# Performance work log

Measured on AMD Instinct MI355X. Metric: run time of the kernel, lower is better.

The kernel has to match this reference:

```python
import jax, jax.numpy as jnp
import numpy as np

DIM = 768
N_HEADS = 12
HEAD_DIM = DIM // N_HEADS
BATCH = 2
SEQ = 4096


def setup_inputs() -> dict:
    key = jax.random.key(0)
    ks = jax.random.split(key, 9)
    s = 1.0 / np.sqrt(DIM)
    return {
        "x": jax.random.normal(ks[0], (BATCH, SEQ, DIM), dtype=jnp.float32),
        "Wq": jax.random.normal(ks[1], (DIM, DIM), dtype=jnp.float32) * s,
        "bq": jax.random.normal(ks[2], (DIM,), dtype=jnp.float32) * s,
        "Wk": jax.random.normal(ks[3], (DIM, DIM), dtype=jnp.float32) * s,
        "bk": jax.random.normal(ks[4], (DIM,), dtype=jnp.float32) * s,
        "Wv": jax.random.normal(ks[5], (DIM, DIM), dtype=jnp.float32) * s,
        "bv": jax.random.normal(ks[6], (DIM,), dtype=jnp.float32) * s,
        "Wo": jax.random.normal(ks[7], (DIM, DIM), dtype=jnp.float32) * s,
        "bo": jax.random.normal(ks[8], (DIM,), dtype=jnp.float32) * s,
    }


def reference(x, Wq, bq, Wk, bk, Wv, bv, Wo, bo):
    B, S, D = x.shape
    scale = 1.0 / np.sqrt(HEAD_DIM).astype(np.float32)
    # projections: [B,S,D] -> [B,H,S,Hd]
    def split_heads(t):
        return t.reshape(B, S, N_HEADS, HEAD_DIM).transpose(0, 2, 1, 3)
    q = split_heads(x @ Wq + bq)
    k = split_heads(x @ Wk + bk)
    v = split_heads(x @ Wv + bv)
    # full score matrix [B,H,S,S] as in the original (memory-bound)
    scores = jnp.einsum("bhqd,bhkd->bhqk", q, k) * scale
    attn = jax.nn.softmax(scores, axis=-1)
    out = jnp.einsum("bhqk,bhkd->bhqd", attn, v)
    out = out.transpose(0, 2, 1, 3).reshape(B, S, D)
    return out @ Wo + bo
```

## Files before the change

### kernel.cpp

```cpp
#include <hip/hip_runtime.h>
#include <hip/hip_bf16.h>
#include <math.h>

#define D_MODEL 768
#define NH 12
#define HD 64
#define BATCH 2
#define SEQ 4096
#define NROWS (BATCH * SEQ)

#define QSCALE 0.18033688011112042f

typedef __attribute__((ext_vector_type(8))) short short8;
typedef __attribute__((ext_vector_type(4))) short short4v;
typedef __attribute__((ext_vector_type(4))) float f32x4;
typedef __attribute__((ext_vector_type(16))) float f32x16;

__device__ inline unsigned short f2bf(float f) {
    __hip_bfloat16 h = __float2bfloat16(f);
    return *reinterpret_cast<unsigned short*>(&h);
}

__device__ __forceinline__ void async_ld16(const unsigned short* g, unsigned short* l) {
    __builtin_amdgcn_global_load_lds(
        (const __attribute__((address_space(1))) void*)g,
        (__attribute__((address_space(3))) void*)l, 16, 0, 0);
}

__global__ __launch_bounds__(256) void convert_x_k(
    const float* __restrict__ x, unsigned short* __restrict__ xb)
{
    size_t i = ((size_t)blockIdx.x * 256 + threadIdx.x) * 8;
    float4 a = *(const float4*)(x + i);
    float4 b = *(const float4*)(x + i + 4);
    short8 o;
    o[0] = (short)f2bf(a.x); o[1] = (short)f2bf(a.y);
    o[2] = (short)f2bf(a.z); o[3] = (short)f2bf(a.w);
    o[4] = (short)f2bf(b.x); o[5] = (short)f2bf(b.y);
    o[6] = (short)f2bf(b.z); o[7] = (short)f2bf(b.w);
    *(short8*)(xb + i) = o;
}

__global__ __launch_bounds__(256) void convert_wt_k(
    const float* __restrict__ Wq, const float* __restrict__ Wk,
    const float* __restrict__ Wv, const float* __restrict__ Wo,
    unsigned short* __restrict__ wt)
{
    const float* W = (blockIdx.z == 0) ? Wq : (blockIdx.z == 1) ? Wk
                   : (blockIdx.z == 2) ? Wv : Wo;
    unsigned short* dst = wt + (size_t)blockIdx.z * D_MODEL * D_MODEL;
    __shared__ float tile[64][65];
    const int k0 = blockIdx.x * 64, n0 = blockIdx.y * 64;
    const int t = threadIdx.x;
    const int r = t >> 2, seg = t & 3;
    const float* src = W + (size_t)(k0 + r) * D_MODEL + n0 + seg * 16;
    #pragma unroll
    for (int i = 0; i < 4; ++i) {
        float4 v = *(const float4*)(src + i * 4);
        tile[r][seg * 16 + i * 4 + 0] = v.x;
        tile[r][seg * 16 + i * 4 + 1] = v.y;
        tile[r][seg * 16 + i * 4 + 2] = v.z;
        tile[r][seg * 16 + i * 4 + 3] = v.w;
    }
    __syncthreads();
    unsigned short* d = dst + (size_t)(n0 + r) * D_MODEL + k0 + seg * 16;
    short8 o0, o1;
    #pragma unroll
    for (int j = 0; j < 8; ++j) o0[j] = (short)f2bf(tile[seg * 16 + j][r]);
    #pragma unroll
    for (int j = 0; j < 8; ++j) o1[j] = (short)f2bf(tile[seg * 16 + 8 + j][r]);
    *(short8*)(d) = o0;
    *(short8*)(d + 8) = o1;
}

__global__ __launch_bounds__(256) void qkv_mfma_k(
    const unsigned short* __restrict__ xb,
    const unsigned short* __restrict__ wt,
    const float* __restrict__ bq, const float* __restrict__ bk,
    const float* __restrict__ bv,
    unsigned short* __restrict__ qb,
    unsigned short* __restrict__ kb,
    unsigned short* __restrict__ vtb)
{
    __shared__ unsigned short As[128][64];
    __shared__ unsigned short Bs[64][64];
    const int z = blockIdx.z;
    const unsigned short* Wt = wt + (size_t)z * D_MODEL * D_MODEL;
    const float* bias = (z == 0) ? bq : (z == 1) ? bk : bv;
    const int t = threadIdx.x;
    const int w = t >> 6, lane = t & 63, quad = lane >> 4, col = lane & 15;
    const int r0 = blockIdx.x * 128;
    const int c0 = blockIdx.y * 64;

    f32x4 acc[2][4] = {};

    for (int kk = 0; kk < D_MODEL; kk += 64) {
        __syncthreads();
        #pragma unroll
        for (int j = 0; j < 4; ++j) {
            int c = (w * 4 + j) * 64 + lane;
            async_ld16(xb + (size_t)(r0 + (c >> 3)) * D_MODEL + kk + (c & 7) * 8,
                       &As[0][0] + (size_t)c * 8);
        }
        #pragma unroll
        for (int j = 0; j < 2; ++j) {
            int c = (w * 2 + j) * 64 + lane;
            async_ld16(Wt + (size_t)(c0 + (c >> 3)) * D_MODEL + kk + (c & 7) * 8,
                       &Bs[0][0] + (size_t)c * 8);
        }
        __syncthreads();
        #pragma unroll
        for (int ks = 0; ks < 2; ++ks) {
            short8 af[2], bf[4];
            af[0] = *(const short8*)&As[w * 32 + col][ks * 32 + quad * 8];
            af[1] = *(const short8*)&As[w * 32 + 16 + col][ks * 32 + quad * 8];
            #pragma unroll
            for (int nt = 0; nt < 4; ++nt)
                bf[nt] = *(const short8*)&Bs[nt * 16 + col][ks * 32 + quad * 8];
            #pragma unroll
            for (int mt = 0; mt < 2; ++mt)
                #pragma unroll
                for (int nt = 0; nt < 4; ++nt)
                    acc[mt][nt] = __builtin_amdgcn_mfma_f32_16x16x32_bf16(
                        af[mt], bf[nt], acc[mt][nt], 0, 0, 0);
        }
    }

    const int h = blockIdx.y;
    #pragma unroll
    for (int nt = 0; nt < 4; ++nt) {
        const float bv_ = bias[c0 + nt * 16 + col];
        const int hd = nt * 16 + col;
        #pragma unroll
        for (int mt = 0; mt < 2; ++mt) {
            #pragma unroll
            for (int reg = 0; reg < 4; ++reg) {
                int r = r0 + w * 32 + mt * 16 + quad * 4 + reg;
                int b = r >> 12, s = r & (SEQ - 1);
                float val = acc[mt][nt][reg] + bv_;
                size_t bh = (size_t)(b * NH + h);
                if (z == 0)
                    qb[(bh * SEQ + s) * HD + hd] = f2bf(val * QSCALE);
                else if (z == 1)
                    kb[(bh * SEQ + s) * HD + hd] = f2bf(val);
                else
                    vtb[(bh * HD + hd) * SEQ + s] = f2bf(val);
            }
        }
    }
}

__global__ __launch_bounds__(256) void out_mfma_k(
    const unsigned short* __restrict__ ab,
    const unsigned short* __restrict__ wot,
    const float* __restrict__ bo,
    float* __restrict__ out)
{
    __shared__ unsigned short As[128][64];
    __shared__ unsigned short Bs[64][64];
    const int t = threadIdx.x;
    const int w = t >> 6, lane = t & 63, quad = lane >> 4, col = lane & 15;
    const int r0 = blockIdx.x * 128;
    const int c0 = blockIdx.y * 64;

    f32x4 acc[2][4] = {};

    for (int kk = 0; kk < D_MODEL; kk += 64) {
        __syncthreads();
        #pragma unroll
        for (int j = 0; j < 4; ++j) {
            int c = (w * 4 + j) * 64 + lane;
            async_ld16(ab + (size_t)(r0 + (c >> 3)) * D_MODEL + kk + (c & 7) * 8,
                       &As[0][0] + (size_t)c * 8);
        }
        #pragma unroll
        for (int j = 0; j < 2; ++j) {
            int c = (w * 2 + j) * 64 + lane;
            async_ld16(wot + (size_t)(c0 + (c >> 3)) * D_MODEL + kk + (c & 7) * 8,
                       &Bs[0][0] + (size_t)c * 8);
        }
        __syncthreads();
        #pragma unroll
        for (int ks = 0; ks < 2; ++ks) {
            short8 af[2], bf[4];
            af[0] = *(const short8*)&As[w * 32 + col][ks * 32 + quad * 8];
            af[1] = *(const short8*)&As[w * 32 + 16 + col][ks * 32 + quad * 8];
            #pragma unroll
            for (int nt = 0; nt < 4; ++nt)
                bf[nt] = *(const short8*)&Bs[nt * 16 + col][ks * 32 + quad * 8];
            #pragma unroll
            for (int mt = 0; mt < 2; ++mt)
                #pragma unroll
                for (int nt = 0; nt < 4; ++nt)
                    acc[mt][nt] = __builtin_amdgcn_mfma_f32_16x16x32_bf16(
                        af[mt], bf[nt], acc[mt][nt], 0, 0, 0);
        }
    }

    #pragma unroll
    for (int nt = 0; nt < 4; ++nt) {
        const float bv_ = bo[c0 + nt * 16 + col];
        #pragma unroll
        for (int mt = 0; mt < 2; ++mt) {
            #pragma unroll
            for (int reg = 0; reg < 4; ++reg) {
                int r = r0 + w * 32 + mt * 16 + quad * 4 + reg;
                out[(size_t)r * D_MODEL + c0 + nt * 16 + col] = acc[mt][nt][reg] + bv_;
            }
        }
    }
}

__global__ __launch_bounds__(256) void flash_mfma_k(
    const unsigned short* __restrict__ qb,
    const unsigned short* __restrict__ kb,
    const unsigned short* __restrict__ vtb,
    unsigned short* __restrict__ ab)
{
    __shared__ unsigned short Ks[64][66];
    __shared__ unsigned short Vts[64][66];
    __shared__ unsigned short Ps[4][32][66];

    const int t = threadIdx.x;
    const int w = t >> 6, lane = t & 63;
    const int l31 = lane & 31, hi = lane >> 5;
    const int q0 = blockIdx.x * 128;
    const int h = blockIdx.y, b = blockIdx.z;
    const size_t bh = (size_t)b * NH + h;
    const unsigned short* qg = qb + bh * SEQ * HD;
    const unsigned short* kg = kb + bh * SEQ * HD;
    const unsigned short* vg = vtb + bh * HD * SEQ;

    short8 qf[4];
    {
        const unsigned short* src = qg + (size_t)(q0 + w * 32 + l31) * HD + hi * 8;
        #pragma unroll
        for (int ks = 0; ks < 4; ++ks)
            qf[ks] = *(const short8*)(src + ks * 16);
    }

    f32x16 oacc[2] = {};
    float lsum = 0.f;
    const int srow = lane, sseg = w;

    for (int kt = 0; kt < SEQ; kt += 64) {
        const unsigned short* kp = kg + (size_t)(kt + srow) * HD + sseg * 16;
        short8 kr0 = *(const short8*)(kp);
        short8 kr1 = *(const short8*)(kp + 8);
        const unsigned short* vp = vg + (size_t)srow * SEQ + kt + sseg * 16;
        short8 vr0 = *(const short8*)(vp);
        short8 vr1 = *(const short8*)(vp + 8);
        __syncthreads();
        *(short8*)&Ks[srow][sseg * 16]      = kr0;
        *(short8*)&Ks[srow][sseg * 16 + 8]  = kr1;
        *(short8*)&Vts[srow][sseg * 16]     = vr0;
        *(short8*)&Vts[srow][sseg * 16 + 8] = vr1;
        __syncthreads();

        #pragma unroll
        for (int kti = 0; kti < 2; ++kti) {
            f32x16 s = {};
            #pragma unroll
            for (int ks = 0; ks < 4; ++ks) {
                short8 kf = *(const short8*)&Ks[kti * 32 + l31][ks * 16 + hi * 8];
                s = __builtin_amdgcn_mfma_f32_32x32x16_bf16(kf, qf[ks], s, 0, 0, 0);
            }
            #pragma unroll
            for (int rq = 0; rq < 4; ++rq) {
                float p0 = __builtin_amdgcn_exp2f(s[rq * 4 + 0]);
                float p1 = __builtin_amdgcn_exp2f(s[rq * 4 + 1]);
                float p2 = __builtin_amdgcn_exp2f(s[rq * 4 + 2]);
                float p3 = __builtin_amdgcn_exp2f(s[rq * 4 + 3]);
                lsum += (p0 + p1) + (p2 + p3);
                short4v pk;
                pk[0] = (short)f2bf(p0);
                pk[1] = (short)f2bf(p1);
                pk[2] = (short)f2bf(p2);
                pk[3] = (short)f2bf(p3);
                *(short4v*)&Ps[w][l31][kti * 32 + rq * 8 + hi * 4] = pk;
            }
        }

        #pragma unroll
        for (int ks = 0; ks < 4; ++ks) {
            short8 pf = *(const short8*)&Ps[w][l31][ks * 16 + hi * 8];
            #pragma unroll
            for (int dt = 0; dt < 2; ++dt) {
                short8 vf = *(const short8*)&Vts[dt * 32 + l31][ks * 16 + hi * 8];
                oacc[dt] = __builtin_amdgcn_mfma_f32_32x32x16_bf16(
                    vf, pf, oacc[dt], 0, 0, 0);
            }
        }
    }

    lsum += __shfl_xor(lsum, 32);
    float inv = 1.0f / lsum;
    int s = q0 + w * 32 + l31;
    unsigned short* dst = ab + ((size_t)b * SEQ + s) * D_MODEL + h * HD;
    #pragma unroll
    for (int dt = 0; dt < 2; ++dt) {
        #pragma unroll
        for (int rq = 0; rq < 4; ++rq) {
            short4v o4;
            o4[0] = (short)f2bf(oacc[dt][rq * 4 + 0] * inv);
            o4[1] = (short)f2bf(oacc[dt][rq * 4 + 1] * inv);
            o4[2] = (short)f2bf(oacc[dt][rq * 4 + 2] * inv);
            o4[3] = (short)f2bf(oacc[dt][rq * 4 + 3] * inv);
            *(short4v*)(dst + dt * 32 + rq * 8 + hi * 4) = o4;
        }
    }
}

extern "C" void kernel_launch(void* const* d_in, const int* in_sizes, int n_in,
                              void* d_out, int out_size, void* d_ws, size_t ws_size,
                              hipStream_t stream)
{
    const float* x  = (const float*)d_in[0];
    const float* Wq = (const float*)d_in[1];
    const float* bq = (const float*)d_in[2];
    const float* Wk = (const float*)d_in[3];
    const float* bk = (const float*)d_in[4];
    const float* Wv = (const float*)d_in[5];
    const float* bv = (const float*)d_in[6];
    const float* Wo = (const float*)d_in[7];
    const float* bo = (const float*)d_in[8];
    float* out = (float*)d_out;

    const size_t n_x  = (size_t)NROWS * D_MODEL;
    const size_t n_w  = (size_t)D_MODEL * D_MODEL;
    unsigned short* xb  = (unsigned short*)d_ws;
    unsigned short* wt  = xb + n_x;
    unsigned short* qb  = wt + 4 * n_w;
    unsigned short* kb  = qb + n_x;
    unsigned short* vtb = kb + n_x;
    unsigned short* ab  = vtb + n_x;
    const size_t need = ((size_t)4 * n_x + 4 * n_w + n_x) * sizeof(unsigned short);
    if (ws_size < need) return;

    convert_x_k<<<dim3((int)(n_x / 2048)), 256, 0, stream>>>(x, xb);
    convert_wt_k<<<dim3(12, 12, 4), 256, 0, stream>>>(Wq, Wk, Wv, Wo, wt);
    qkv_mfma_k<<<dim3(NROWS / 128, D_MODEL / 64, 3), 256, 0, stream>>>(
        xb, wt, bq, bk, bv, qb, kb, vtb);
    flash_mfma_k<<<dim3(SEQ / 128, NH, BATCH), 256, 0, stream>>>(qb, kb, vtb, ab);
    out_mfma_k<<<dim3(NROWS / 128, D_MODEL / 64), 256, 0, stream>>>(
        ab, wt + 3 * n_w, bo, out);
}
```

Baseline: 320.1 us.

## Keep softmax probabilities in registers via permlane32 swap and prefetch K/V tiles

Removes the shared-memory round trip for the P matrix in the flash attention kernel. Probabilities are now packed with v_cvt_pk_bf16_f32 and redistributed across lanes with permlane32_swap straight into MFMA operand registers. It also register-prefetches the next K/V tile while the current one is in use and raises wave priority around the MFMA blocks. This saves LDS traffic and one barrier-dependent store/load per tile, at the cost of more register pressure and reliance on the exact MFMA lane layout being correct.

```diff
diff --git a/kernel.cpp b/kernel.cpp
--- a/kernel.cpp
+++ b/kernel.cpp
@@ -15,10 +15,21 @@
 typedef __attribute__((ext_vector_type(4))) short short4v;
 typedef __attribute__((ext_vector_type(4))) float f32x4;
 typedef __attribute__((ext_vector_type(16))) float f32x16;
+typedef __attribute__((ext_vector_type(4))) unsigned int uint4v;
 
 __device__ inline unsigned short f2bf(float f) {
     __hip_bfloat16 h = __float2bfloat16(f);
     return *reinterpret_cast<unsigned short*>(&h);
+}
+
+__device__ __forceinline__ unsigned int cvtpk_bf16(float lo, float hi) {
+    unsigned int d;
+    asm("v_cvt_pk_bf16_f32 %0, %1, %2" : "=v"(d) : "v"(lo), "v"(hi));
+    return d;
+}
+
+__device__ __forceinline__ short8 u4_as_s8(uint4v u) {
+    return *reinterpret_cast<short8*>(&u);
 }
 
 __device__ __forceinline__ void async_ld16(const unsigned short* g, unsigned short* l) {
@@ -219,7 +230,6 @@
 {
     __shared__ unsigned short Ks[64][66];
     __shared__ unsigned short Vts[64][66];
-    __shared__ unsigned short Ps[4][32][66];
 
     const int t = threadIdx.x;
     const int w = t >> 6, lane = t & 63;
@@ -243,54 +253,82 @@
     float lsum = 0.f;
     const int srow = lane, sseg = w;
 
+    short8 kr0, kr1, vr0, vr1;
+    {
+        const unsigned short* kp = kg + (size_t)srow * HD + sseg * 16;
+        kr0 = *(const short8*)(kp);
+        kr1 = *(const short8*)(kp + 8);
+        const unsigned short* vp = vg + (size_t)srow * SEQ + sseg * 16;
+        vr0 = *(const short8*)(vp);
+        vr1 = *(const short8*)(vp + 8);
+    }
+
     for (int kt = 0; kt < SEQ; kt += 64) {
-        const unsigned short* kp = kg + (size_t)(kt + srow) * HD + sseg * 16;
-        short8 kr0 = *(const short8*)(kp);
-        short8 kr1 = *(const short8*)(kp + 8);
-        const unsigned short* vp = vg + (size_t)srow * SEQ + kt + sseg * 16;
-        short8 vr0 = *(const short8*)(vp);
-        short8 vr1 = *(const short8*)(vp + 8);
         __syncthreads();
         *(short8*)&Ks[srow][sseg * 16]      = kr0;
         *(short8*)&Ks[srow][sseg * 16 + 8]  = kr1;
         *(short8*)&Vts[srow][sseg * 16]     = vr0;
         *(short8*)&Vts[srow][sseg * 16 + 8] = vr1;
-        __syncthreads();
-
+        if (kt + 64 < SEQ) {
+            const unsigned short* kp = kg + (size_t)(kt + 64 + srow) * HD + sseg * 16;
+            kr0 = *(const short8*)(kp);
+            kr1 = *(const short8*)(kp + 8);
+            const unsigned short* vp = vg + (size_t)srow * SEQ + kt + 64 + sseg * 16;
+            vr0 = *(const short8*)(vp);
+            vr1 = *(const short8*)(vp + 8);
+        }
+        __syncthreads();
+
+        short8 pf[4];
         #pragma unroll
         for (int kti = 0; kti < 2; ++kti) {
             f32x16 s = {};
+            __builtin_amdgcn_s_setprio(1);
             #pragma unroll
             for (int ks = 0; ks < 4; ++ks) {
                 short8 kf = *(const short8*)&Ks[kti * 32 + l31][ks * 16 + hi * 8];
                 s = __builtin_amdgcn_mfma_f32_32x32x16_bf16(kf, qf[ks], s, 0, 0, 0);
             }
-            #pragma unroll
-            for (int rq = 0; rq < 4; ++rq) {
-                float p0 = __builtin_amdgcn_exp2f(s[rq * 4 + 0]);
-                float p1 = __builtin_amdgcn_exp2f(s[rq * 4 + 1]);
-                float p2 = __builtin_amdgcn_exp2f(s[rq * 4 + 2]);
-                float p3 = __builtin_amdgcn_exp2f(s[rq * 4 + 3]);
-                lsum += (p0 + p1) + (p2 + p3);
-                short4v pk;
-                pk[0] = (short)f2bf(p0);
-                pk[1] = (short)f2bf(p1);
-                pk[2] = (short)f2bf(p2);
-                pk[3] = (short)f2bf(p3);
-                *(short4v*)&Ps[w][l31][kti * 32 + rq * 8 + hi * 4] = pk;
-            }
-        }
-
+            __builtin_amdgcn_s_setprio(0);
+            float p[16];
+            #pragma unroll
+            for (int r = 0; r < 16; ++r)
+                p[r] = __builtin_amdgcn_exp2f(s[r]);
+            lsum += (((p[0] + p[1]) + (p[2] + p[3])) + ((p[4] + p[5]) + (p[6] + p[7])))
+                  + (((p[8] + p[9]) + (p[10] + p[11])) + ((p[12] + p[13]) + (p[14] + p[15])));
+            unsigned int c01 = cvtpk_bf16(p[0],  p[1]);
+            unsigned int c45 = cvtpk_bf16(p[4],  p[5]);
+            unsigned int c23 = cvtpk_bf16(p[2],  p[3]);
+            unsigned int c67 = cvtpk_bf16(p[6],  p[7]);
+            unsigned int c89 = cvtpk_bf16(p[8],  p[9]);
+            unsigned int cCD = cvtpk_bf16(p[12], p[13]);
+            unsigned int cAB = cvtpk_bf16(p[10], p[11]);
+            unsigned int cEF = cvtpk_bf16(p[14], p[15]);
+            auto r0 = __builtin_amdgcn_permlane32_swap((int)c01, (int)c45, false, false);
+            auto r1 = __builtin_amdgcn_permlane32_swap((int)c23, (int)c67, false, false);
+            auto r2 = __builtin_amdgcn_permlane32_swap((int)c89, (int)cCD, false, false);
+            auto r3 = __builtin_amdgcn_permlane32_swap((int)cAB, (int)cEF, false, false);
+            uint4v u0, u1;
+            u0[0] = (unsigned int)r0[0]; u0[1] = (unsigned int)r1[0];
+            u0[2] = (unsigned int)r0[1]; u0[3] = (unsigned int)r1[1];
+            u1[0] = (unsigned int)r2[0]; u1[1] = (unsigned int)r3[0];
+            u1[2] = (unsigned int)r2[1]; u1[3] = (unsigned int)r3[1];
+            pf[kti * 2 + 0] = u4_as_s8(u0);
+            pf[kti * 2 + 1] = u4_as_s8(u1);
+        }
+
+        __builtin_amdgcn_s_setprio(1);
         #pragma unroll
         for (int ks = 0; ks < 4; ++ks) {
-            short8 pf = *(const short8*)&Ps[w][l31][ks * 16 + hi * 8];
+            short8 pfk = pf[ks];
             #pragma unroll
             for (int dt = 0; dt < 2; ++dt) {
                 short8 vf = *(const short8*)&Vts[dt * 32 + l31][ks * 16 + hi * 8];
                 oacc[dt] = __builtin_amdgcn_mfma_f32_32x32x16_bf16(
-                    vf, pf, oacc[dt], 0, 0, 0);
+                    vf, pfk, oacc[dt], 0, 0, 0);
             }
         }
+        __builtin_amdgcn_s_setprio(0);
     }
 
     lsum += __shfl_xor(lsum, 32);
```

New measurement: 306.3 us. 4.3% less time.
